# Optimization experiments

Hardware: AMD Instinct MI355X
Metric: run time of the kernel (lower is better)

Reference implementation:

```python
import jax, jax.numpy as jnp
import numpy as np

MARGIN = 0.3  # init_kwargs
EPS = 1e-12   # torch F.normalize eps


def _pairwise_dist(f):
    # Euclidean cdist via the stable quadratic expansion; f is [B, D].
    sq = jnp.sum(f * f, axis=1)                      # [B]
    d2 = sq[:, None] + sq[None, :] - 2.0 * (f @ f.T)  # [B, B]
    d2 = jnp.maximum(d2, 0.0)
    # safe sqrt: zero distance (diagonal / duplicates) -> 0 with zero grad
    pos = d2 > 0.0
    return jnp.sqrt(jnp.where(pos, d2, 1.0)) * pos


def reference(features, labels):
    B = features.shape[0]
    norm = jnp.linalg.norm(features, axis=1, keepdims=True)
    f = features / jnp.maximum(norm, EPS)            # F.normalize(dim=1)

    dist = _pairwise_dist(f)                         # [B, B]
    mask = labels[:, None] == labels[None, :]        # positives (incl. self)

    pos_count = jnp.sum(mask, axis=1)                # [B], >= 1 (self)
    has_pos = pos_count > 1                          # needs another positive
    has_neg = pos_count < B                          # at least one negative
    valid = has_pos & has_neg

    # mean over positive distances (includes the self-distance 0, as in torch code)
    mean_pos = jnp.sum(dist * mask, axis=1) / pos_count.astype(dist.dtype)  # [B]

    # semi-hard negatives: negatives with dist > mean positive dist
    sh_mask = (~mask) & (dist > mean_pos[:, None])   # [B, B]
    has_sh = jnp.any(sh_mask, axis=1)
    min_sh = jnp.min(jnp.where(sh_mask, dist, jnp.inf), axis=1)
    min_sh = jnp.where(has_sh, min_sh, 0.0)          # guard inf for invalid rows

    contrib = valid & has_sh
    per_anchor = jax.nn.relu(mean_pos - min_sh + MARGIN)
    loss_sum = jnp.sum(jnp.where(contrib, per_anchor, 0.0))
    count = jnp.sum(contrib)
    return jnp.where(count > 0, loss_sum / count.astype(dist.dtype), 0.0)


def setup_inputs() -> dict:
    key = jax.random.key(0)
    k1, k2 = jax.random.split(key)
    features = jax.random.normal(k1, (8192, 512), dtype=jnp.float32)
    labels = jax.random.randint(k2, (8192,), 0, 128, dtype=jnp.int64)
    return {"features": features, "labels": labels}
```

## Files before the change

kernel.cpp:

```cpp
#include <hip/hip_runtime.h>
#include <math.h>

#define EPS_N 1e-12f
#define MARGIN 0.3f
#define INF_BITS 0x7f800000u
#define NCLS 128
#define D 512
#define PADR 256

typedef __attribute__((ext_vector_type(8))) short short8;
typedef __attribute__((ext_vector_type(4))) float float4v;

__device__ __forceinline__ unsigned short f2bf(float f) {
    unsigned u = __float_as_uint(f);
    u += 0x7fff + ((u >> 16) & 1);
    return (unsigned short)(u >> 16);
}
__device__ __forceinline__ void gl16(const void* g, void* l) {
    __builtin_amdgcn_global_load_lds((const __attribute__((address_space(1))) void*)g,
                                     (__attribute__((address_space(3))) void*)l, 16, 0, 0);
}

__global__ __launch_bounds__(1024) void k_bucket(const int* __restrict__ lab, int Bn,
        int* __restrict__ pos, int* __restrict__ labp,
        int* __restrict__ cstart_g, int* __restrict__ ccnt_g,
        float* __restrict__ meanpos, float* __restrict__ pcinv,
        int* __restrict__ poscnt, unsigned* __restrict__ minbits) {
    __shared__ int cnt[NCLS], cs[NCLS + 1], off[NCLS], sa[NCLS], sb[NCLS];
    int tid = threadIdx.x;
    if (tid < NCLS) cnt[tid] = 0;
    __syncthreads();
    for (int i = tid; i < Bn; i += 1024) atomicAdd(&cnt[lab[i] & (NCLS - 1)], 1);
    __syncthreads();
    if (tid < NCLS) sa[tid] = cnt[tid];
    __syncthreads();
    int* src = sa; int* dst = sb;
    for (int ofs = 1; ofs < NCLS; ofs <<= 1) {
        if (tid < NCLS) dst[tid] = src[tid] + ((tid >= ofs) ? src[tid - ofs] : 0);
        __syncthreads();
        int* t = src; src = dst; dst = t;
    }
    if (tid < NCLS) {
        int ex = src[tid] - cnt[tid];
        cs[tid] = ex;
        off[tid] = ex;
        cstart_g[tid] = ex;
        ccnt_g[tid] = cnt[tid];
    }
    if (tid == 0) cs[NCLS] = Bn;
    __syncthreads();
    for (int p = tid; p < Bn; p += 1024) {
        int lo = 0, hi = NCLS - 1;
        #pragma unroll
        for (int s = 0; s < 7; ++s) {
            int mid = (lo + hi + 1) >> 1;
            if (cs[mid] <= p) lo = mid; else hi = mid - 1;
        }
        int l = lo, m = cnt[l];
        labp[p] = l;
        poscnt[p] = m;
        pcinv[p] = 1.0f / (float)m;
        meanpos[p] = 0.f;
        minbits[p] = INF_BITS;
    }
    for (int i = tid; i < Bn; i += 1024) {
        int l = lab[i] & (NCLS - 1);
        pos[i] = atomicAdd(&off[l], 1);
    }
}

__global__ __launch_bounds__(256) void k_normalize(const float* __restrict__ x,
        const int* __restrict__ pos, unsigned short* __restrict__ fh,
        float* __restrict__ sqp) {
    int w = threadIdx.x >> 6, L = threadIdx.x & 63;
    int row = blockIdx.x * 4 + w;
    const float* xr = x + (size_t)row * D + L * 8;
    float4 a = *(const float4*)xr;
    float4 b = *(const float4*)(xr + 4);
    float ss = a.x * a.x;
    ss = fmaf(a.y, a.y, ss); ss = fmaf(a.z, a.z, ss); ss = fmaf(a.w, a.w, ss);
    ss = fmaf(b.x, b.x, ss); ss = fmaf(b.y, b.y, ss);
    ss = fmaf(b.z, b.z, ss); ss = fmaf(b.w, b.w, ss);
    #pragma unroll
    for (int off = 32; off; off >>= 1) ss += __shfl_xor(ss, off, 64);
    float inv = 1.0f / fmaxf(sqrtf(ss), EPS_N);
    int prow = pos[row];
    if (L == 0) sqp[prow] = ss * inv * inv;
    ushort4 h0, h1;
    h0.x = f2bf(a.x * inv); h0.y = f2bf(a.y * inv);
    h0.z = f2bf(a.z * inv); h0.w = f2bf(a.w * inv);
    h1.x = f2bf(b.x * inv); h1.y = f2bf(b.y * inv);
    h1.z = f2bf(b.z * inv); h1.w = f2bf(b.w * inv);
    unsigned short* dst = fh + (size_t)prow * D + L * 8;
    *(ushort4*)dst = h0;
    *(ushort4*)(dst + 4) = h1;
}

__global__ __launch_bounds__(256) void k_posband3(
    const unsigned short* __restrict__ fh, const float* __restrict__ sqp,
    const int* __restrict__ labp, const int* __restrict__ cstart_g,
    const int* __restrict__ ccnt_g, float* __restrict__ meanpos, int Bn)
{
    __shared__ unsigned short SA[16 * 128];
    __shared__ unsigned short SB[128 * 128];
    __shared__ float sqr[16], rs[16];
    __shared__ int labr[16];
    __shared__ float sqc[128];
    __shared__ int labc[128];

    const int r0 = blockIdx.x * 16;
    const int tid = threadIdx.x, w = tid >> 6, L = tid & 63;
    const int lm = L & 15, ls = L >> 4;
    const int srow = L >> 4;
    const int sseg = L & 15;

    if (tid < 16) {
        labr[tid] = labp[r0 + tid];
        sqr[tid]  = sqp[r0 + tid];
        rs[tid]   = 0.f;
    }
    __syncthreads();
    const int c0 = cstart_g[labr[0]];
    const int c1 = cstart_g[labr[15]] + ccnt_g[labr[15]];

    for (int cc0 = c0; cc0 < c1; cc0 += 128) {
        __syncthreads();
        if (tid < 128) {
            int q = cc0 + tid;
            if (q < Bn) { sqc[tid] = sqp[q]; labc[tid] = labp[q]; }
            else        { sqc[tid] = 0.f;    labc[tid] = -1; }
        }
        float4v acc[2];
        acc[0] = (float4v){0.f, 0.f, 0.f, 0.f};
        acc[1] = (float4v){0.f, 0.f, 0.f, 0.f};

        for (int k0 = 0; k0 < D; k0 += 128) {
            __syncthreads();
            {
                int rmat = w * 4 + srow;
                int seg = sseg ^ (rmat & 15);
                gl16(fh + (size_t)(r0 + rmat) * D + k0 + seg * 8, &SA[(w * 4) * 128]);
            }
            #pragma unroll
            for (int it = 0; it < 8; ++it) {
                int rmat = it * 16 + w * 4 + srow;
                int seg = sseg ^ (rmat & 15);
                gl16(fh + (size_t)(cc0 + rmat) * D + k0 + seg * 8,
                     &SB[(size_t)(it * 16 + w * 4) * 128]);
            }
            __syncthreads();
            #pragma unroll
            for (int h = 0; h < 4; ++h) {
                int ra = lm;
                short8 af = *(const short8*)&SA[ra * 128 + (((h * 4 + ls) ^ (ra & 15))) * 8];
                #pragma unroll
                for (int ct = 0; ct < 2; ++ct) {
                    int rb = w * 32 + ct * 16 + lm;
                    short8 bf = *(const short8*)&SB[rb * 128 + (((h * 4 + ls) ^ (rb & 15))) * 8];
                    acc[ct] = __builtin_amdgcn_mfma_f32_16x16x32_bf16(af, bf, acc[ct], 0, 0, 0);
                }
            }
        }
        #pragma unroll
        for (int v = 0; v < 4; ++v) {
            int ri = ls * 4 + v;
            int p = r0 + ri;
            int lr = labr[ri];
            float sr = sqr[ri];
            float sum = 0.f;
            #pragma unroll
            for (int ct = 0; ct < 2; ++ct) {
                int ci = w * 32 + ct * 16 + lm;
                int q = cc0 + ci;
                float d2 = sr + sqc[ci] - 2.0f * acc[ct][v];
                float dd = (d2 > 0.f) ? sqrtf(d2) : 0.f;
                sum += ((labc[ci] == lr) && (q != p)) ? dd : 0.f;
            }
            #pragma unroll
            for (int off = 8; off; off >>= 1) sum += __shfl_xor(sum, off, 64);
            if (lm == 0) atomicAdd(&rs[ri], sum);
        }
    }
    __syncthreads();
    if (tid < 16 && rs[tid] != 0.f) atomicAdd(&meanpos[r0 + tid], rs[tid]);
}

#define BKG 64

__global__ __launch_bounds__(256, 4) void k_minsh_mfma(
    const unsigned short* __restrict__ fh, const float* __restrict__ sqp,
    const int* __restrict__ labp, const float* __restrict__ meanpos,
    const float* __restrict__ pcinv, unsigned* __restrict__ minbits)
{
    int t = blockIdx.x;
    int rq = (int)((sqrtf(8.0f * (float)t + 1.0f) - 1.0f) * 0.5f);
    while ((rq + 1) * (rq + 2) / 2 <= t) ++rq;
    while (rq * (rq + 1) / 2 > t) --rq;
    int cq = t - rq * (rq + 1) / 2;
    const int i0 = cq * 128, j0 = rq * 128;
    const bool diag = (i0 == j0);

    __shared__ unsigned short LA[2][128 * BKG];
    __shared__ float s_mp2r[128], s_mp2c[128], s_sqr[128], s_sqc[128];
    __shared__ int s_labr[128], s_labc[128];

    const int tid = threadIdx.x;
    const int w = tid >> 6, L = tid & 63;

    if (tid < 128) {
        float mp = meanpos[i0 + tid] * pcinv[i0 + tid];
        s_mp2r[tid] = mp * mp;
        s_sqr[tid]  = sqp[i0 + tid];
        s_labr[tid] = labp[i0 + tid];
    } else {
        int q = tid - 128;
        float mp = meanpos[j0 + q] * pcinv[j0 + q];
        s_mp2c[q] = mp * mp;
        s_sqc[q]  = sqp[j0 + q];
        s_labc[q] = labp[j0 + q];
    }

    const unsigned short* msrc = fh + (size_t)((w < 2) ? i0 : j0) * D;
    unsigned short* mylds = &LA[(w < 2) ? 0 : 1][(w & 1) * 64 * BKG];
    const int srow = L >> 3;
    const int sseg = L & 7;

    float4v acc[4][4];
    #pragma unroll
    for (int a = 0; a < 4; ++a)
        #pragma unroll
        for (int bq = 0; bq < 4; ++bq) acc[a][bq] = (float4v){0.f, 0.f, 0.f, 0.f};

    const int rw = (w >> 1) * 64, cw = (w & 1) * 64;
    const int lm = L & 15, ls = L >> 4;

    for (int k0 = 0; k0 < D; k0 += BKG) {
        __syncthreads();
        #pragma unroll
        for (int it = 0; it < 8; ++it) {
            int rmat = (w & 1) * 64 + it * 8 + srow;
            int seg = sseg ^ (rmat & 7);
            gl16(msrc + (size_t)rmat * D + k0 + seg * 8, mylds + it * 512);
        }
        __syncthreads();
        #pragma unroll
        for (int h = 0; h < 2; ++h) {
            short8 ah[4], bh[4];
            #pragma unroll
            for (int mi = 0; mi < 4; ++mi) {
                int r = rw + mi * 16 + lm;
                int slot = r * 8 + ((h * 4 + ls) ^ (r & 7));
                ah[mi] = *(const short8*)&LA[0][slot * 8];
            }
            #pragma unroll
            for (int ni = 0; ni < 4; ++ni) {
                int cc = cw + ni * 16 + lm;
                int slot = cc * 8 + ((h * 4 + ls) ^ (cc & 7));
                bh[ni] = *(const short8*)&LA[1][slot * 8];
            }
            #pragma unroll
            for (int ni = 0; ni < 4; ++ni)
                #pragma unroll
                for (int mi = 0; mi < 4; ++mi)
                    acc[mi][ni] = __builtin_amdgcn_mfma_f32_16x16x32_bf16(ah[mi], bh[ni], acc[mi][ni], 0, 0, 0);
        }
    }

    const float INFF = __uint_as_float(INF_BITS);
    float sc[4], mp2c[4];
    int lc[4];
    #pragma unroll
    for (int ni = 0; ni < 4; ++ni) {
        int cl = cw + ni * 16 + lm;
        sc[ni]   = s_sqc[cl];
        mp2c[ni] = s_mp2c[cl];
        lc[ni]   = s_labc[cl];
    }
    float vminc[4];
    #pragma unroll
    for (int ni = 0; ni < 4; ++ni) vminc[ni] = INFF;

    #pragma unroll
    for (int mi = 0; mi < 4; ++mi) {
        #pragma unroll
        for (int v = 0; v < 4; ++v) {
            int rl = rw + mi * 16 + ls * 4 + v;
            float mp2r = s_mp2r[rl];
            float sr   = s_sqr[rl];
            int   li   = s_labr[rl];
            float vminr = INFF;
            #pragma unroll
            for (int ni = 0; ni < 4; ++ni) {
                float d2 = fmaf(-2.0f, acc[mi][ni][v], sr + sc[ni]);
                bool neq = (li != lc[ni]);
                vminr     = fminf(vminr,     (neq && d2 > mp2r)     ? d2 : INFF);
                vminc[ni] = fminf(vminc[ni], (neq && d2 > mp2c[ni]) ? d2 : INFF);
            }
            #pragma unroll
            for (int off = 8; off; off >>= 1)
                vminr = fminf(vminr, __shfl_xor(vminr, off, 64));
            if (lm == 0 && __float_as_uint(vminr) != INF_BITS)
                atomicMin(&minbits[i0 + rl], __float_as_uint(vminr));
        }
    }
    if (!diag) {
        #pragma unroll
        for (int ni = 0; ni < 4; ++ni) {
            float vc = vminc[ni];
            vc = fminf(vc, __shfl_xor(vc, 16, 64));
            vc = fminf(vc, __shfl_xor(vc, 32, 64));
            if (ls == 0 && __float_as_uint(vc) != INF_BITS)
                atomicMin(&minbits[j0 + cw + ni * 16 + lm], __float_as_uint(vc));
        }
    }
}

__global__ __launch_bounds__(1024) void k_finish(const float* __restrict__ meanpos,
        const float* __restrict__ pcinv, const int* __restrict__ poscnt,
        const unsigned* __restrict__ minbits, float* __restrict__ out, int Bn) {
    float lsum = 0.f; int lcnt = 0;
    for (int i = threadIdx.x; i < Bn; i += 1024) {
        int pc = poscnt[i];
        bool valid = (pc > 1) && (pc < Bn);
        unsigned mb = minbits[i];
        if (valid && mb != INF_BITS) {
            float v = fmaf(meanpos[i], pcinv[i], MARGIN - sqrtf(__uint_as_float(mb)));
            lsum += (v > 0.f) ? v : 0.f;
            lcnt += 1;
        }
    }
    __shared__ float ssum[16]; __shared__ int scnt[16];
    int lane = threadIdx.x & 63, wid = threadIdx.x >> 6;
    #pragma unroll
    for (int off = 32; off; off >>= 1) {
        lsum += __shfl_down(lsum, off, 64);
        lcnt += __shfl_down(lcnt, off, 64);
    }
    if (lane == 0) { ssum[wid] = lsum; scnt[wid] = lcnt; }
    __syncthreads();
    if (threadIdx.x == 0) {
        float s = 0.f; int c = 0;
        #pragma unroll
        for (int q = 0; q < 16; ++q) { s += ssum[q]; c += scnt[q]; }
        out[0] = (c > 0) ? s / (float)c : 0.f;
    }
}

extern "C" void kernel_launch(void* const* d_in, const int* in_sizes, int n_in,
                              void* d_out, int out_size, void* d_ws, size_t ws_size,
                              hipStream_t stream) {
    const float* x = (const float*)d_in[0];
    const int* lab = (const int*)d_in[1];
    int Bn = in_sizes[1];

    size_t nd = (size_t)(Bn + PADR) * D;
    unsigned short* fh = (unsigned short*)d_ws;
    float* sqp        = (float*)(fh + nd);
    float* meanpos    = sqp + Bn;
    float* pcinv      = meanpos + Bn;
    int* poscnt       = (int*)(pcinv + Bn);
    unsigned* minbits = (unsigned*)(poscnt + Bn);
    int* pos          = (int*)(minbits + Bn);
    int* labp         = pos + Bn;
    int* cstart_g     = labp + Bn;
    int* ccnt_g       = cstart_g + NCLS;

    k_bucket<<<1, 1024, 0, stream>>>(lab, Bn, pos, labp, cstart_g, ccnt_g,
                                     meanpos, pcinv, poscnt, minbits);
    k_normalize<<<Bn / 4, 256, 0, stream>>>(x, pos, fh, sqp);
    k_posband3<<<Bn / 16, 256, 0, stream>>>(fh, sqp, labp, cstart_g, ccnt_g,
                                            meanpos, Bn);
    int nb = Bn / 128;
    int T = nb * (nb + 1) / 2;
    k_minsh_mfma<<<T, 256, 0, stream>>>(fh, sqp, labp, meanpos, pcinv, minbits);
    k_finish<<<1, 1024, 0, stream>>>(meanpos, pcinv, poscnt, minbits,
                                     (float*)d_out, Bn);
}
```

Baseline: 159.4 us.

## Compute positive-distance sums per class block instead of per 16-row band

Replaces the band kernel, which gave each 16-row block the whole column range covering its labels, with one block per class. Each block computes only the within-class 128x128 Gram tiles and reuses the A tile as B on diagonal tiles. This removes redundant loads of columns outside the class, as well as the label compares and the global atomics. The trade-off is only 128 blocks on a large GPU and uneven work when class sizes differ.

```diff
diff --git a/kernel.cpp b/kernel.cpp
--- a/kernel.cpp
+++ b/kernel.cpp
@@ -96,93 +96,106 @@
     *(ushort4*)(dst + 4) = h1;
 }
 
-__global__ __launch_bounds__(256) void k_posband3(
+__global__ __launch_bounds__(256) void k_posclass(
     const unsigned short* __restrict__ fh, const float* __restrict__ sqp,
-    const int* __restrict__ labp, const int* __restrict__ cstart_g,
-    const int* __restrict__ ccnt_g, float* __restrict__ meanpos, int Bn)
+    const int* __restrict__ cstart_g, const int* __restrict__ ccnt_g,
+    float* __restrict__ meanpos)
 {
-    __shared__ unsigned short SA[16 * 128];
+    const int c = blockIdx.x;
+    const int s = cstart_g[c], n = ccnt_g[c];
+    if (n <= 1) return;
+
+    __shared__ unsigned short SA[128 * 128];
     __shared__ unsigned short SB[128 * 128];
-    __shared__ float sqr[16], rs[16];
-    __shared__ int labr[16];
-    __shared__ float sqc[128];
-    __shared__ int labc[128];
-
-    const int r0 = blockIdx.x * 16;
+    __shared__ float sqr_sh[128], sqs[128], rs[128];
+
     const int tid = threadIdx.x, w = tid >> 6, L = tid & 63;
     const int lm = L & 15, ls = L >> 4;
-    const int srow = L >> 4;
-    const int sseg = L & 15;
-
-    if (tid < 16) {
-        labr[tid] = labp[r0 + tid];
-        sqr[tid]  = sqp[r0 + tid];
-        rs[tid]   = 0.f;
-    }
-    __syncthreads();
-    const int c0 = cstart_g[labr[0]];
-    const int c1 = cstart_g[labr[15]] + ccnt_g[labr[15]];
-
-    for (int cc0 = c0; cc0 < c1; cc0 += 128) {
+
+    for (int rb = 0; rb < n; rb += 128) {
+        const int nr = min(128, n - rb);
         __syncthreads();
         if (tid < 128) {
-            int q = cc0 + tid;
-            if (q < Bn) { sqc[tid] = sqp[q]; labc[tid] = labp[q]; }
-            else        { sqc[tid] = 0.f;    labc[tid] = -1; }
-        }
-        float4v acc[2];
-        acc[0] = (float4v){0.f, 0.f, 0.f, 0.f};
-        acc[1] = (float4v){0.f, 0.f, 0.f, 0.f};
-
-        for (int k0 = 0; k0 < D; k0 += 128) {
+            rs[tid] = 0.f;
+            sqr_sh[tid] = (tid < nr) ? sqp[s + rb + tid] : 0.f;
+        }
+        for (int cb = 0; cb < n; cb += 128) {
+            const int m = min(128, n - cb);
+            const bool same = (rb == cb);
             __syncthreads();
-            {
-                int rmat = w * 4 + srow;
-                int seg = sseg ^ (rmat & 15);
-                gl16(fh + (size_t)(r0 + rmat) * D + k0 + seg * 8, &SA[(w * 4) * 128]);
-            }
-            #pragma unroll
-            for (int it = 0; it < 8; ++it) {
-                int rmat = it * 16 + w * 4 + srow;
-                int seg = sseg ^ (rmat & 15);
-                gl16(fh + (size_t)(cc0 + rmat) * D + k0 + seg * 8,
-                     &SB[(size_t)(it * 16 + w * 4) * 128]);
-            }
-            __syncthreads();
-            #pragma unroll
-            for (int h = 0; h < 4; ++h) {
-                int ra = lm;
-                short8 af = *(const short8*)&SA[ra * 128 + (((h * 4 + ls) ^ (ra & 15))) * 8];
-                #pragma unroll
-                for (int ct = 0; ct < 2; ++ct) {
-                    int rb = w * 32 + ct * 16 + lm;
-                    short8 bf = *(const short8*)&SB[rb * 128 + (((h * 4 + ls) ^ (rb & 15))) * 8];
-                    acc[ct] = __builtin_amdgcn_mfma_f32_16x16x32_bf16(af, bf, acc[ct], 0, 0, 0);
+            if (tid < 128) sqs[tid] = (tid < m) ? sqp[s + cb + tid] : 0.f;
+
+            float4v acc[8][2];
+            #pragma unroll
+            for (int rt = 0; rt < 8; ++rt)
+                #pragma unroll
+                for (int ct = 0; ct < 2; ++ct) acc[rt][ct] = (float4v){0.f, 0.f, 0.f, 0.f};
+
+            for (int k0 = 0; k0 < D; k0 += 128) {
+                __syncthreads();
+                #pragma unroll
+                for (int q = 0; q < 8; ++q) {
+                    int slot = tid + 256 * q;
+                    int r = slot >> 4;
+                    int u = (slot & 15) ^ (r & 15);
+                    if (r < nr)
+                        gl16(fh + (size_t)(s + rb + r) * D + k0 + u * 8,
+                             &SA[(w * 64 + 256 * q) * 8]);
                 }
-            }
-        }
-        #pragma unroll
-        for (int v = 0; v < 4; ++v) {
-            int ri = ls * 4 + v;
-            int p = r0 + ri;
-            int lr = labr[ri];
-            float sr = sqr[ri];
-            float sum = 0.f;
-            #pragma unroll
-            for (int ct = 0; ct < 2; ++ct) {
-                int ci = w * 32 + ct * 16 + lm;
-                int q = cc0 + ci;
-                float d2 = sr + sqc[ci] - 2.0f * acc[ct][v];
-                float dd = (d2 > 0.f) ? sqrtf(d2) : 0.f;
-                sum += ((labc[ci] == lr) && (q != p)) ? dd : 0.f;
-            }
-            #pragma unroll
-            for (int off = 8; off; off >>= 1) sum += __shfl_xor(sum, off, 64);
-            if (lm == 0) atomicAdd(&rs[ri], sum);
-        }
-    }
-    __syncthreads();
-    if (tid < 16 && rs[tid] != 0.f) atomicAdd(&meanpos[r0 + tid], rs[tid]);
+                if (!same) {
+                    #pragma unroll
+                    for (int q = 0; q < 8; ++q) {
+                        int slot = tid + 256 * q;
+                        int r = slot >> 4;
+                        int u = (slot & 15) ^ (r & 15);
+                        if (r < m)
+                            gl16(fh + (size_t)(s + cb + r) * D + k0 + u * 8,
+                                 &SB[(w * 64 + 256 * q) * 8]);
+                    }
+                }
+                __syncthreads();
+                const unsigned short* Bb = same ? SA : SB;
+                #pragma unroll
+                for (int h = 0; h < 4; ++h) {
+                    short8 bf[2];
+                    #pragma unroll
+                    for (int ct = 0; ct < 2; ++ct) {
+                        int cr = w * 32 + ct * 16 + lm;
+                        bf[ct] = *(const short8*)&Bb[cr * 128 + (((h * 4 + ls) ^ (cr & 15))) * 8];
+                    }
+                    #pragma unroll
+                    for (int rt = 0; rt < 8; ++rt) {
+                        int ar = rt * 16 + lm;
+                        short8 af = *(const short8*)&SA[ar * 128 + (((h * 4 + ls) ^ (ar & 15))) * 8];
+                        #pragma unroll
+                        for (int ct = 0; ct < 2; ++ct)
+                            acc[rt][ct] = __builtin_amdgcn_mfma_f32_16x16x32_bf16(af, bf[ct], acc[rt][ct], 0, 0, 0);
+                    }
+                }
+            }
+            #pragma unroll
+            for (int rt = 0; rt < 8; ++rt) {
+                #pragma unroll
+                for (int v = 0; v < 4; ++v) {
+                    int ri = rt * 16 + ls * 4 + v;
+                    float sr = sqr_sh[ri];
+                    float sum = 0.f;
+                    #pragma unroll
+                    for (int ct = 0; ct < 2; ++ct) {
+                        int ci = w * 32 + ct * 16 + lm;
+                        float d2 = sr + sqs[ci] - 2.0f * acc[rt][ct][v];
+                        bool ok = (ri < nr) && (ci < m) && (rb + ri != cb + ci) && (d2 > 0.f);
+                        sum += ok ? sqrtf(d2) : 0.f;
+                    }
+                    #pragma unroll
+                    for (int off = 8; off; off >>= 1) sum += __shfl_xor(sum, off, 64);
+                    if (lm == 0 && sum != 0.f) atomicAdd(&rs[ri], sum);
+                }
+            }
+        }
+        __syncthreads();
+        if (tid < nr) meanpos[s + rb + tid] = rs[tid];
+    }
 }
 
 #define BKG 64
@@ -368,8 +381,7 @@
     k_bucket<<<1, 1024, 0, stream>>>(lab, Bn, pos, labp, cstart_g, ccnt_g,
                                      meanpos, pcinv, poscnt, minbits);
     k_normalize<<<Bn / 4, 256, 0, stream>>>(x, pos, fh, sqp);
-    k_posband3<<<Bn / 16, 256, 0, stream>>>(fh, sqp, labp, cstart_g, ccnt_g,
-                                            meanpos, Bn);
+    k_posclass<<<NCLS, 256, 0, stream>>>(fh, sqp, cstart_g, ccnt_g, meanpos);
     int nb = Bn / 128;
     int T = nb * (nb + 1) / 2;
     k_minsh_mfma<<<T, 256, 0, stream>>>(fh, sqp, labp, meanpos, pcinv, minbits);
```

New measurement: 159.1 us. About the same (-0.2%).
